# Performance work log

Hardware: AMD Instinct MI355X
Metric: run time of the kernel (lower is better)

The kernel has to match this reference:

```python
import jax, jax.numpy as jnp
from jax import lax
import numpy as np

B, S, H, V = 128, 512, 1024, 128


def setup_inputs() -> dict:
    key = jax.random.key(0)
    ks = jax.random.split(key, 8)
    s = 1.0 / np.sqrt(H)
    return {
        "x": jax.random.randint(ks[0], (B, S), 0, V, dtype=jnp.int32),
        "emb": jax.random.normal(ks[1], (V, H), dtype=jnp.float32),
        "W_ih": jax.random.uniform(ks[2], (H, H), jnp.float32, -s, s),
        "W_hh": jax.random.uniform(ks[3], (H, H), jnp.float32, -s, s),
        "b_ih": jax.random.uniform(ks[4], (H,), jnp.float32, -s, s),
        "b_hh": jax.random.uniform(ks[5], (H,), jnp.float32, -s, s),
        "W_fc": jax.random.uniform(ks[6], (V, H), jnp.float32, -s, s),
        "b_fc": jax.random.uniform(ks[7], (V,), jnp.float32, -s, s),
    }


def reference(x, emb, W_ih, W_hh, b_ih, b_hh, W_fc, b_fc):
    # Embedding lookup: [B, S, H]
    xe = emb[x]
    # Batched input projection for all timesteps (one big GEMM), fold in both biases
    xp = jnp.einsum("bsh,ih->bsi", xe, W_ih) + (b_ih + b_hh)  # [B, S, H]
    h0 = jnp.zeros((x.shape[0], W_hh.shape[0]), dtype=xp.dtype)

    def step(h, xt):  # xt: [B, H]
        h_new = jnp.tanh(xt + h @ W_hh.T)
        return h_new, None

    hT, _ = lax.scan(step, h0, jnp.swapaxes(xp, 0, 1))  # scan over time
    # Final-step linear: [B, V]
    return hT @ W_fc.T + b_fc
```

## Files before the change

kernel.cpp:

```cpp
#include <hip/hip_runtime.h>
#include <hip/hip_bf16.h>
#include <stdint.h>

#define Bb 128
#define Ss 512
#define Hh 1024
#define Vv 128

#define GROUPS 8
#define WPG 16
#define MB 16
#define NCOL 64

typedef __attribute__((ext_vector_type(8))) short short8;
typedef __attribute__((ext_vector_type(4))) float float4v;

static __device__ __forceinline__ short f2bf(float f) {
    union { float f; uint32_t u; } x; x.f = f;
    uint32_t r = x.u + 0x7FFFu + ((x.u >> 16) & 1u);
    return (short)(r >> 16);
}
static __device__ __forceinline__ float bf2f(uint16_t b) {
    union { uint32_t u; float f; } x; x.u = ((uint32_t)b) << 16;
    return x.f;
}

__global__ void k_prep(const float* __restrict__ emb, const float* __restrict__ Wih,
                       const float* __restrict__ bih, const float* __restrict__ bhh,
                       float* __restrict__ P) {
    int v = blockIdx.x >> 2;
    int i = ((blockIdx.x & 3) << 8) + threadIdx.x;
    const float4v* e4 = (const float4v*)(emb + v * Hh);
    const float4v* w4 = (const float4v*)(Wih + i * Hh);
    float acc = 0.f;
    #pragma unroll 4
    for (int h = 0; h < Hh / 4; ++h) {
        float4v a = e4[h], b = w4[h];
        acc += a[0]*b[0] + a[1]*b[1] + a[2]*b[2] + a[3]*b[3];
    }
    P[v * Hh + i] = acc + bih[i] + bhh[i];
}

__launch_bounds__(256, 1)
__global__ void k_rnn(const int* __restrict__ x, const float* __restrict__ Whh,
                      const float* __restrict__ P,
                      uint16_t* __restrict__ h0, uint16_t* __restrict__ h1,
                      uint32_t* __restrict__ ctr) {
    __shared__ int    x_lds[Ss][MB];
    __shared__ float  P_lds[Vv][NCOL];
    __shared__ float4v red[4][4][64];

    const int g    = blockIdx.x >> 4;
    const int w    = blockIdx.x & 15;
    const int r0   = g * MB;
    const int n0   = w * NCOL;
    const int tid  = threadIdx.x;
    const int lane = tid & 63;
    const int q    = tid >> 6;

    for (int l = tid; l < Ss * MB; l += 256) {
        int t = l >> 4, r = l & 15;
        x_lds[t][r] = x[(r0 + r) * Ss + t];
    }
    for (int l = tid; l < Vv * NCOL; l += 256) {
        int v = l >> 6, c = l & 63;
        P_lds[v][c] = P[v * Hh + n0 + c];
    }

    short8 bf[4][8];
    {
        const int n_lane = lane & 15;
        const int k_base = q * 256 + ((lane >> 4) << 3);
        #pragma unroll
        for (int nt = 0; nt < 4; ++nt) {
            const float* wrow = Whh + (size_t)(n0 + nt * 16 + n_lane) * Hh;
            #pragma unroll
            for (int s = 0; s < 8; ++s) {
                const float* src = wrow + k_base + s * 32;
                short8 tmp;
                #pragma unroll
                for (int e = 0; e < 8; ++e) tmp[e] = f2bf(src[e]);
                bf[nt][s] = tmp;
            }
        }
    }
    __syncthreads();

    uint32_t* myctr = ctr + g * 64;
    const int row_base = (lane >> 4) << 2;
    const int c_lane   = lane & 15;

    for (int t = 0; t < Ss; ++t) {
        float4v acc0 = {0.f,0.f,0.f,0.f}, acc1 = {0.f,0.f,0.f,0.f};
        float4v acc2 = {0.f,0.f,0.f,0.f}, acc3 = {0.f,0.f,0.f,0.f};

        if (t > 0) {
            const uint16_t* hin = (t & 1) ? h1 : h0;
            const uint16_t* arow = hin + (size_t)(r0 + c_lane) * Hh + q * 256 + ((lane >> 4) << 3);
            short8 a0,a1,a2,a3,a4,a5,a6,a7;
            asm volatile(
                "global_load_dwordx4 %0, %8, off sc0 sc1\n\t"
                "global_load_dwordx4 %1, %8, off offset:64 sc0 sc1\n\t"
                "global_load_dwordx4 %2, %8, off offset:128 sc0 sc1\n\t"
                "global_load_dwordx4 %3, %8, off offset:192 sc0 sc1\n\t"
                "global_load_dwordx4 %4, %8, off offset:256 sc0 sc1\n\t"
                "global_load_dwordx4 %5, %8, off offset:320 sc0 sc1\n\t"
                "global_load_dwordx4 %6, %8, off offset:384 sc0 sc1\n\t"
                "global_load_dwordx4 %7, %8, off offset:448 sc0 sc1\n\t"
                "s_waitcnt vmcnt(0)"
                : "=&v"(a0), "=&v"(a1), "=&v"(a2), "=&v"(a3),
                  "=&v"(a4), "=&v"(a5), "=&v"(a6), "=&v"(a7)
                : "v"(arow)
                : "memory");
            #define MM(s, areg) \
                acc0 = __builtin_amdgcn_mfma_f32_16x16x32_bf16(areg, bf[0][s], acc0, 0,0,0); \
                acc1 = __builtin_amdgcn_mfma_f32_16x16x32_bf16(areg, bf[1][s], acc1, 0,0,0); \
                acc2 = __builtin_amdgcn_mfma_f32_16x16x32_bf16(areg, bf[2][s], acc2, 0,0,0); \
                acc3 = __builtin_amdgcn_mfma_f32_16x16x32_bf16(areg, bf[3][s], acc3, 0,0,0);
            MM(0,a0) MM(1,a1) MM(2,a2) MM(3,a3) MM(4,a4) MM(5,a5) MM(6,a6) MM(7,a7)
            #undef MM
        }

        red[q][0][lane] = acc0;
        red[q][1][lane] = acc1;
        red[q][2][lane] = acc2;
        red[q][3][lane] = acc3;
        __syncthreads();

        {
            float4v u = red[0][q][lane];
            u += red[1][q][lane];
            u += red[2][q][lane];
            u += red[3][q][lane];
            uint16_t* hout = ((t + 1) & 1) ? h1 : h0;
            const int pcol = q * 16 + c_lane;
            const int ncol = n0 + pcol;
            int v0i = x_lds[t][row_base + 0], v1i = x_lds[t][row_base + 1];
            int v2i = x_lds[t][row_base + 2], v3i = x_lds[t][row_base + 3];
            uint32_t b0 = (uint16_t)f2bf(tanhf(u[0] + P_lds[v0i][pcol]));
            uint32_t b1 = (uint16_t)f2bf(tanhf(u[1] + P_lds[v1i][pcol]));
            uint32_t b2 = (uint16_t)f2bf(tanhf(u[2] + P_lds[v2i][pcol]));
            uint32_t b3 = (uint16_t)f2bf(tanhf(u[3] + P_lds[v3i][pcol]));
            uint16_t* p0 = hout + (size_t)(r0 + row_base) * Hh + ncol;
            uint16_t* p2 = p0 + 2 * Hh;
            asm volatile(
                "global_store_short %0, %2, off sc0 sc1\n\t"
                "global_store_short %0, %3, off offset:2048 sc0 sc1\n\t"
                "global_store_short %1, %4, off sc0 sc1\n\t"
                "global_store_short %1, %5, off offset:2048 sc0 sc1\n\t"
                "s_waitcnt vmcnt(0)"
                :: "v"(p0), "v"(p2), "v"(b0), "v"(b1), "v"(b2), "v"(b3)
                : "memory");
        }

        __syncthreads();
        if (tid == 0) {
            __hip_atomic_fetch_add(myctr, 1u, __ATOMIC_RELAXED, __HIP_MEMORY_SCOPE_AGENT);
            const uint32_t target = (uint32_t)(WPG * (t + 1));
            while (__hip_atomic_load(myctr, __ATOMIC_RELAXED, __HIP_MEMORY_SCOPE_AGENT) < target)
                __builtin_amdgcn_s_sleep(1);
        }
        __syncthreads();
    }
}

__global__ void k_fc(const uint16_t* __restrict__ hT, const float* __restrict__ Wfc,
                     const float* __restrict__ bfc, float* __restrict__ out) {
    int bb = (blockIdx.x >> 3) << 4;
    int vb = (blockIdx.x & 7) << 4;
    int b  = bb + (threadIdx.x >> 4);
    int v  = vb + (threadIdx.x & 15);
    const uint16_t* hrow = hT + (size_t)b * Hh;
    const float*    wrow = Wfc + (size_t)v * Hh;
    float acc = 0.f;
    #pragma unroll 4
    for (int i = 0; i < Hh; i += 4) {
        float4v wv = *(const float4v*)(wrow + i);
        acc += bf2f(hrow[i + 0]) * wv[0] + bf2f(hrow[i + 1]) * wv[1]
             + bf2f(hrow[i + 2]) * wv[2] + bf2f(hrow[i + 3]) * wv[3];
    }
    out[(size_t)b * Vv + v] = acc + bfc[v];
}

extern "C" void kernel_launch(void* const* d_in, const int* in_sizes, int n_in,
                              void* d_out, int out_size, void* d_ws, size_t ws_size,
                              hipStream_t stream) {
    const int*   x   = (const int*)d_in[0];
    const float* emb = (const float*)d_in[1];
    const float* Wih = (const float*)d_in[2];
    const float* Whh = (const float*)d_in[3];
    const float* bih = (const float*)d_in[4];
    const float* bhh = (const float*)d_in[5];
    const float* Wfc = (const float*)d_in[6];
    const float* bfc = (const float*)d_in[7];
    float* out = (float*)d_out;

    char* ws = (char*)d_ws;
    float*    P   = (float*)ws;
    uint16_t* h0  = (uint16_t*)(ws + (512 << 10));
    uint16_t* h1  = (uint16_t*)(ws + (768 << 10));
    uint32_t* ctr = (uint32_t*)(ws + (1024 << 10));

    hipMemsetAsync(ctr, 0, 4096, stream);
    k_prep<<<512, 256, 0, stream>>>(emb, Wih, bih, bhh, P);
    k_rnn<<<128, 256, 0, stream>>>(x, Whh, P, h0, h1, ctr);
    k_fc<<<64, 256, 0, stream>>>(h0, Wfc, bfc, out);
}
```

Measured before the change: 1.837 ms.

## Replace per-step atomic counter barrier with per-wave flag polling

The per-timestep group barrier is replaced. Before, thread 0 of each block did an atomic add plus a sleep-poll loop, wrapped in two block-wide __syncthreads. Now each wave publishes its own step flag right after its h stores complete. Before loading the previous hidden state, every wave polls all 64 flags of its group with one coalesced load and a wave-wide vote. This removes the block barriers, the atomics and the sleep latency from the serial recurrence, at the cost of more global polling traffic and correctness that relies on store ordering and on the flags also protecting reuse of the LDS reduction buffer.

```diff
diff --git a/kernel.cpp b/kernel.cpp
--- a/kernel.cpp
+++ b/kernel.cpp
@@ -45,7 +45,7 @@
 __global__ void k_rnn(const int* __restrict__ x, const float* __restrict__ Whh,
                       const float* __restrict__ P,
                       uint16_t* __restrict__ h0, uint16_t* __restrict__ h1,
-                      uint32_t* __restrict__ ctr) {
+                      uint32_t* __restrict__ flags) {
     __shared__ int    x_lds[Ss][MB];
     __shared__ float  P_lds[Vv][NCOL];
     __shared__ float4v red[4][4][64];
@@ -86,7 +86,10 @@
     }
     __syncthreads();
 
-    uint32_t* myctr = ctr + g * 64;
+    uint32_t* grp_flags = flags + (g << 6);
+    uint32_t* myflag    = grp_flags + ((w << 2) + q);
+    const uint32_t* pollp = grp_flags + lane;
+
     const int row_base = (lane >> 4) << 2;
     const int c_lane   = lane & 15;
 
@@ -95,6 +98,15 @@
         float4v acc2 = {0.f,0.f,0.f,0.f}, acc3 = {0.f,0.f,0.f,0.f};
 
         if (t > 0) {
+            const uint32_t tgt = (uint32_t)t;
+            for (;;) {
+                uint32_t fv;
+                asm volatile("global_load_dword %0, %1, off sc0 sc1\n\t"
+                             "s_waitcnt vmcnt(0)"
+                             : "=v"(fv) : "v"(pollp) : "memory");
+                if (__all((int)(fv >= tgt))) break;
+            }
+
             const uint16_t* hin = (t & 1) ? h1 : h0;
             const uint16_t* arow = hin + (size_t)(r0 + c_lane) * Hh + q * 256 + ((lane >> 4) << 3);
             short8 a0,a1,a2,a3,a4,a5,a6,a7;
@@ -143,24 +155,18 @@
             uint32_t b3 = (uint16_t)f2bf(tanhf(u[3] + P_lds[v3i][pcol]));
             uint16_t* p0 = hout + (size_t)(r0 + row_base) * Hh + ncol;
             uint16_t* p2 = p0 + 2 * Hh;
+            const uint32_t tp1 = (uint32_t)(t + 1);
             asm volatile(
                 "global_store_short %0, %2, off sc0 sc1\n\t"
                 "global_store_short %0, %3, off offset:2048 sc0 sc1\n\t"
                 "global_store_short %1, %4, off sc0 sc1\n\t"
                 "global_store_short %1, %5, off offset:2048 sc0 sc1\n\t"
-                "s_waitcnt vmcnt(0)"
-                :: "v"(p0), "v"(p2), "v"(b0), "v"(b1), "v"(b2), "v"(b3)
+                "s_waitcnt vmcnt(0)\n\t"
+                "global_store_dword %6, %7, off sc0 sc1"
+                :: "v"(p0), "v"(p2), "v"(b0), "v"(b1), "v"(b2), "v"(b3),
+                   "v"(myflag), "v"(tp1)
                 : "memory");
         }
-
-        __syncthreads();
-        if (tid == 0) {
-            __hip_atomic_fetch_add(myctr, 1u, __ATOMIC_RELAXED, __HIP_MEMORY_SCOPE_AGENT);
-            const uint32_t target = (uint32_t)(WPG * (t + 1));
-            while (__hip_atomic_load(myctr, __ATOMIC_RELAXED, __HIP_MEMORY_SCOPE_AGENT) < target)
-                __builtin_amdgcn_s_sleep(1);
-        }
-        __syncthreads();
     }
 }
 
@@ -196,13 +202,13 @@
     float* out = (float*)d_out;
 
     char* ws = (char*)d_ws;
-    float*    P   = (float*)ws;
-    uint16_t* h0  = (uint16_t*)(ws + (512 << 10));
-    uint16_t* h1  = (uint16_t*)(ws + (768 << 10));
-    uint32_t* ctr = (uint32_t*)(ws + (1024 << 10));
-
-    hipMemsetAsync(ctr, 0, 4096, stream);
+    float*    P     = (float*)ws;
+    uint16_t* h0    = (uint16_t*)(ws + (512 << 10));
+    uint16_t* h1    = (uint16_t*)(ws + (768 << 10));
+    uint32_t* flags = (uint32_t*)(ws + (1024 << 10));
+
+    hipMemsetAsync(flags, 0, 4096, stream);
     k_prep<<<512, 256, 0, stream>>>(emb, Wih, bih, bhh, P);
-    k_rnn<<<128, 256, 0, stream>>>(x, Whh, P, h0, h1, ctr);
+    k_rnn<<<128, 256, 0, stream>>>(x, Whh, P, h0, h1, flags);
     k_fc<<<64, 256, 0, stream>>>(h0, Wfc, bfc, out);
 }
```

New measurement: 2.353 ms. 28.1% more time.

## Replace atomic counter barrier with step-tagged hidden state polling and fast tanh

Applied to the files above, without the earlier changes.

Replaces the per-timestep atomic counter barrier across the 16 workgroups of a batch group with flag-in-data synchronization. Each hidden value is stored as a 32-bit word carrying the bf16 value plus a timestep tag, and readers spin on the loaded data until every tag matches. This removes the two __syncthreads plus the atomic round trip per step, and double-buffers the LDS reduction scratch. The exchange doubles hidden-state traffic, adds a spin budget that can silently proceed with stale data, and swaps tanhf for an exp2/rcp approximation. The tags are never reset between calls, which risks stale matches on repeated runs.

```diff
diff --git a/kernel.cpp b/kernel.cpp
--- a/kernel.cpp
+++ b/kernel.cpp
@@ -14,6 +14,7 @@
 
 typedef __attribute__((ext_vector_type(8))) short short8;
 typedef __attribute__((ext_vector_type(4))) float float4v;
+typedef __attribute__((ext_vector_type(4))) unsigned int uint4v;
 
 static __device__ __forceinline__ short f2bf(float f) {
     union { float f; uint32_t u; } x; x.f = f;
@@ -23,6 +24,10 @@
 static __device__ __forceinline__ float bf2f(uint16_t b) {
     union { uint32_t u; float f; } x; x.u = ((uint32_t)b) << 16;
     return x.f;
+}
+static __device__ __forceinline__ float ftanh(float x) {
+    float e = __builtin_amdgcn_exp2f(x * 2.885390082f);
+    return 1.0f - 2.0f * __builtin_amdgcn_rcpf(e + 1.0f);
 }
 
 __global__ void k_prep(const float* __restrict__ emb, const float* __restrict__ Wih,
@@ -44,11 +49,10 @@
 __launch_bounds__(256, 1)
 __global__ void k_rnn(const int* __restrict__ x, const float* __restrict__ Whh,
                       const float* __restrict__ P,
-                      uint16_t* __restrict__ h0, uint16_t* __restrict__ h1,
-                      uint32_t* __restrict__ ctr) {
-    __shared__ int    x_lds[Ss][MB];
-    __shared__ float  P_lds[Vv][NCOL];
-    __shared__ float4v red[4][4][64];
+                      uint32_t* __restrict__ h0u, uint32_t* __restrict__ h1u) {
+    __shared__ int     x_lds[Ss][MB];
+    __shared__ float   P_lds[Vv][NCOL];
+    __shared__ float4v red[2][4][4][64];
 
     const int g    = blockIdx.x >> 4;
     const int w    = blockIdx.x & 15;
@@ -86,98 +90,136 @@
     }
     __syncthreads();
 
-    uint32_t* myctr = ctr + g * 64;
     const int row_base = (lane >> 4) << 2;
     const int c_lane   = lane & 15;
+    int budget = 1 << 22;
+
+    const int probe_off = (Hh * (r0 + 15)) + ((q << 2) + ((lane & 15) >> 2)) * 64
+                          + ((lane & 3) << 4);
 
     for (int t = 0; t < Ss; ++t) {
         float4v acc0 = {0.f,0.f,0.f,0.f}, acc1 = {0.f,0.f,0.f,0.f};
         float4v acc2 = {0.f,0.f,0.f,0.f}, acc3 = {0.f,0.f,0.f,0.f};
 
         if (t > 0) {
-            const uint16_t* hin = (t & 1) ? h1 : h0;
-            const uint16_t* arow = hin + (size_t)(r0 + c_lane) * Hh + q * 256 + ((lane >> 4) << 3);
-            short8 a0,a1,a2,a3,a4,a5,a6,a7;
-            asm volatile(
-                "global_load_dwordx4 %0, %8, off sc0 sc1\n\t"
-                "global_load_dwordx4 %1, %8, off offset:64 sc0 sc1\n\t"
-                "global_load_dwordx4 %2, %8, off offset:128 sc0 sc1\n\t"
-                "global_load_dwordx4 %3, %8, off offset:192 sc0 sc1\n\t"
-                "global_load_dwordx4 %4, %8, off offset:256 sc0 sc1\n\t"
-                "global_load_dwordx4 %5, %8, off offset:320 sc0 sc1\n\t"
-                "global_load_dwordx4 %6, %8, off offset:384 sc0 sc1\n\t"
-                "global_load_dwordx4 %7, %8, off offset:448 sc0 sc1\n\t"
-                "s_waitcnt vmcnt(0)"
-                : "=&v"(a0), "=&v"(a1), "=&v"(a2), "=&v"(a3),
-                  "=&v"(a4), "=&v"(a5), "=&v"(a6), "=&v"(a7)
-                : "v"(arow)
-                : "memory");
-            #define MM(s, areg) \
-                acc0 = __builtin_amdgcn_mfma_f32_16x16x32_bf16(areg, bf[0][s], acc0, 0,0,0); \
-                acc1 = __builtin_amdgcn_mfma_f32_16x16x32_bf16(areg, bf[1][s], acc1, 0,0,0); \
-                acc2 = __builtin_amdgcn_mfma_f32_16x16x32_bf16(areg, bf[2][s], acc2, 0,0,0); \
-                acc3 = __builtin_amdgcn_mfma_f32_16x16x32_bf16(areg, bf[3][s], acc3, 0,0,0);
-            MM(0,a0) MM(1,a1) MM(2,a2) MM(3,a3) MM(4,a4) MM(5,a5) MM(6,a6) MM(7,a7)
-            #undef MM
+            const uint32_t tag = (uint32_t)t;
+            const uint32_t* hin = (t & 1) ? h1u : h0u;
+
+            {
+                const uint32_t* pp = hin + probe_off;
+                for (;;) {
+                    uint32_t fv;
+                    asm volatile("global_load_dword %0, %1, off sc0 sc1\n\t"
+                                 "s_waitcnt vmcnt(0)"
+                                 : "=v"(fv) : "v"(pp) : "memory");
+                    if (__all((int)((fv & 0xFFFFu) == tag))) break;
+                    if (--budget <= 0) break;
+                }
+            }
+
+            const uint32_t* arow = hin + (size_t)(r0 + c_lane) * Hh + q * 256
+                                   + ((lane >> 4) << 3);
+            uint4v dd[16];
+            for (;;) {
+                asm volatile(
+                    "global_load_dwordx4 %0, %8, off sc0 sc1\n\t"
+                    "global_load_dwordx4 %1, %8, off offset:16 sc0 sc1\n\t"
+                    "global_load_dwordx4 %2, %8, off offset:128 sc0 sc1\n\t"
+                    "global_load_dwordx4 %3, %8, off offset:144 sc0 sc1\n\t"
+                    "global_load_dwordx4 %4, %8, off offset:256 sc0 sc1\n\t"
+                    "global_load_dwordx4 %5, %8, off offset:272 sc0 sc1\n\t"
+                    "global_load_dwordx4 %6, %8, off offset:384 sc0 sc1\n\t"
+                    "global_load_dwordx4 %7, %8, off offset:400 sc0 sc1"
+                    : "=&v"(dd[0]), "=&v"(dd[1]), "=&v"(dd[2]), "=&v"(dd[3]),
+                      "=&v"(dd[4]), "=&v"(dd[5]), "=&v"(dd[6]), "=&v"(dd[7])
+                    : "v"(arow) : "memory");
+                asm volatile(
+                    "global_load_dwordx4 %0, %8, off offset:512 sc0 sc1\n\t"
+                    "global_load_dwordx4 %1, %8, off offset:528 sc0 sc1\n\t"
+                    "global_load_dwordx4 %2, %8, off offset:640 sc0 sc1\n\t"
+                    "global_load_dwordx4 %3, %8, off offset:656 sc0 sc1\n\t"
+                    "global_load_dwordx4 %4, %8, off offset:768 sc0 sc1\n\t"
+                    "global_load_dwordx4 %5, %8, off offset:784 sc0 sc1\n\t"
+                    "global_load_dwordx4 %6, %8, off offset:896 sc0 sc1\n\t"
+                    "global_load_dwordx4 %7, %8, off offset:912 sc0 sc1\n\t"
+                    "s_waitcnt vmcnt(0)"
+                    : "=&v"(dd[8]), "=&v"(dd[9]), "=&v"(dd[10]), "=&v"(dd[11]),
+                      "=&v"(dd[12]), "=&v"(dd[13]), "=&v"(dd[14]), "=&v"(dd[15])
+                    : "v"(arow) : "memory");
+                uint32_t ok = 1u;
+                #pragma unroll
+                for (int i = 0; i < 16; ++i) ok &= (uint32_t)((dd[i].x & 0xFFFFu) == tag);
+                if (__all((int)ok)) break;
+                if (--budget <= 0) break;
+            }
+
+            #define PK(d0, d1) (((d0) >> 16) | ((d1) & 0xFFFF0000u))
+            #pragma unroll
+            for (int s = 0; s < 8; ++s) {
+                uint4v lo = dd[2 * s], hi = dd[2 * s + 1];
+                uint4v pk = { PK(lo.x, lo.y), PK(lo.z, lo.w),
+                              PK(hi.x, hi.y), PK(hi.z, hi.w) };
+                short8 a;
+                __builtin_memcpy(&a, &pk, 16);
+                acc0 = __builtin_amdgcn_mfma_f32_16x16x32_bf16(a, bf[0][s], acc0, 0,0,0);
+                acc1 = __builtin_amdgcn_mfma_f32_16x16x32_bf16(a, bf[1][s], acc1, 0,0,0);
+                acc2 = __builtin_amdgcn_mfma_f32_16x16x32_bf16(a, bf[2][s], acc2, 0,0,0);
+                acc3 = __builtin_amdgcn_mfma_f32_16x16x32_bf16(a, bf[3][s], acc3, 0,0,0);
+            }
+            #undef PK
         }
 
-        red[q][0][lane] = acc0;
-        red[q][1][lane] = acc1;
-        red[q][2][lane] = acc2;
-        red[q][3][lane] = acc3;
+        const int pb = t & 1;
+        red[pb][q][0][lane] = acc0;
+        red[pb][q][1][lane] = acc1;
+        red[pb][q][2][lane] = acc2;
+        red[pb][q][3][lane] = acc3;
         __syncthreads();
 
         {
-            float4v u = red[0][q][lane];
-            u += red[1][q][lane];
-            u += red[2][q][lane];
-            u += red[3][q][lane];
-            uint16_t* hout = ((t + 1) & 1) ? h1 : h0;
+            float4v u = red[pb][0][q][lane];
+            u += red[pb][1][q][lane];
+            u += red[pb][2][q][lane];
+            u += red[pb][3][q][lane];
+            uint32_t* hout = ((t + 1) & 1) ? h1u : h0u;
             const int pcol = q * 16 + c_lane;
             const int ncol = n0 + pcol;
             int v0i = x_lds[t][row_base + 0], v1i = x_lds[t][row_base + 1];
             int v2i = x_lds[t][row_base + 2], v3i = x_lds[t][row_base + 3];
-            uint32_t b0 = (uint16_t)f2bf(tanhf(u[0] + P_lds[v0i][pcol]));
-            uint32_t b1 = (uint16_t)f2bf(tanhf(u[1] + P_lds[v1i][pcol]));
-            uint32_t b2 = (uint16_t)f2bf(tanhf(u[2] + P_lds[v2i][pcol]));
-            uint32_t b3 = (uint16_t)f2bf(tanhf(u[3] + P_lds[v3i][pcol]));
-            uint16_t* p0 = hout + (size_t)(r0 + row_base) * Hh + ncol;
-            uint16_t* p2 = p0 + 2 * Hh;
-            asm volatile(
-                "global_store_short %0, %2, off sc0 sc1\n\t"
-                "global_store_short %0, %3, off offset:2048 sc0 sc1\n\t"
-                "global_store_short %1, %4, off sc0 sc1\n\t"
-                "global_store_short %1, %5, off offset:2048 sc0 sc1\n\t"
-                "s_waitcnt vmcnt(0)"
-                :: "v"(p0), "v"(p2), "v"(b0), "v"(b1), "v"(b2), "v"(b3)
-                : "memory");
+            const uint32_t t1 = (uint32_t)(t + 1);
+            uint32_t b0 = ((uint32_t)(uint16_t)f2bf(ftanh(u[0] + P_lds[v0i][pcol])) << 16) | t1;
+            uint32_t b1 = ((uint32_t)(uint16_t)f2bf(ftanh(u[1] + P_lds[v1i][pcol])) << 16) | t1;
+            uint32_t b2 = ((uint32_t)(uint16_t)f2bf(ftanh(u[2] + P_lds[v2i][pcol])) << 16) | t1;
+            uint32_t b3 = ((uint32_t)(uint16_t)f2bf(ftanh(u[3] + P_lds[v3i][pcol])) << 16) | t1;
+            uint32_t* p0 = hout + (size_t)(r0 + row_base) * Hh + ncol;
+            asm volatile("global_store_dword %0, %1, off sc0 sc1"
+                         :: "v"(p0),            "v"(b0) : "memory");
+            asm volatile("global_store_dword %0, %1, off sc0 sc1"
+                         :: "v"(p0 + Hh),       "v"(b1) : "memory");
+            asm volatile("global_store_dword %0, %1, off sc0 sc1"
+                         :: "v"(p0 + 2 * Hh),   "v"(b2) : "memory");
+            asm volatile("global_store_dword %0, %1, off sc0 sc1"
+                         :: "v"(p0 + 3 * Hh),   "v"(b3) : "memory");
         }
-
-        __syncthreads();
-        if (tid == 0) {
-            __hip_atomic_fetch_add(myctr, 1u, __ATOMIC_RELAXED, __HIP_MEMORY_SCOPE_AGENT);
-            const uint32_t target = (uint32_t)(WPG * (t + 1));
-            while (__hip_atomic_load(myctr, __ATOMIC_RELAXED, __HIP_MEMORY_SCOPE_AGENT) < target)
-                __builtin_amdgcn_s_sleep(1);
-        }
-        __syncthreads();
-    }
-}
-
-__global__ void k_fc(const uint16_t* __restrict__ hT, const float* __restrict__ Wfc,
+    }
+}
+
+__global__ void k_fc(const uint32_t* __restrict__ hT, const float* __restrict__ Wfc,
                      const float* __restrict__ bfc, float* __restrict__ out) {
     int bb = (blockIdx.x >> 3) << 4;
     int vb = (blockIdx.x & 7) << 4;
     int b  = bb + (threadIdx.x >> 4);
     int v  = vb + (threadIdx.x & 15);
-    const uint16_t* hrow = hT + (size_t)b * Hh;
+    const uint32_t* hrow = hT + (size_t)b * Hh;
     const float*    wrow = Wfc + (size_t)v * Hh;
     float acc = 0.f;
     #pragma unroll 4
     for (int i = 0; i < Hh; i += 4) {
         float4v wv = *(const float4v*)(wrow + i);
-        acc += bf2f(hrow[i + 0]) * wv[0] + bf2f(hrow[i + 1]) * wv[1]
-             + bf2f(hrow[i + 2]) * wv[2] + bf2f(hrow[i + 3]) * wv[3];
+        acc += bf2f((uint16_t)(hrow[i + 0] >> 16)) * wv[0]
+             + bf2f((uint16_t)(hrow[i + 1] >> 16)) * wv[1]
+             + bf2f((uint16_t)(hrow[i + 2] >> 16)) * wv[2]
+             + bf2f((uint16_t)(hrow[i + 3] >> 16)) * wv[3];
     }
     out[(size_t)b * Vv + v] = acc + bfc[v];
 }
@@ -197,12 +239,10 @@
 
     char* ws = (char*)d_ws;
     float*    P   = (float*)ws;
-    uint16_t* h0  = (uint16_t*)(ws + (512 << 10));
-    uint16_t* h1  = (uint16_t*)(ws + (768 << 10));
-    uint32_t* ctr = (uint32_t*)(ws + (1024 << 10));
-
-    hipMemsetAsync(ctr, 0, 4096, stream);
+    uint32_t* h0u = (uint32_t*)(ws + (512 << 10));
+    uint32_t* h1u = (uint32_t*)(ws + (1024 << 10));
+
     k_prep<<<512, 256, 0, stream>>>(emb, Wih, bih, bhh, P);
-    k_rnn<<<128, 256, 0, stream>>>(x, Whh, P, h0, h1, ctr);
-    k_fc<<<64, 256, 0, stream>>>(h0, Wfc, bfc, out);
-}
+    k_rnn<<<128, 256, 0, stream>>>(x, Whh, P, h0u, h1u);
+    k_fc<<<64, 256, 0, stream>>>(h0u, Wfc, bfc, out);
+}
```

Result: slower. 1.908 ms (+3.9%).
